# Optimization experiments

Measured on AMD Instinct MI355X. Metric: run time of the kernel, lower is better.

The kernel has to match this reference:

```python
import jax, jax.numpy as jnp
import numpy as np

SEQ_LEN = 720
PRED_LEN = 720
PERIOD = 24
EMB = 64
P_IN = SEQ_LEN // PERIOD            # 30
P_OUT = -(-PRED_LEN // PERIOD)      # 30 (ceil)
FREQ = EMB // 2 + 1                 # 33
DOM = (SEQ_LEN // PERIOD + 1) * 2 + 10  # 72
RATIO = PRED_LEN / SEQ_LEN          # 1.0


def _clin(z, Wr, Wi, br, bi):
    # complex nn.Linear over last dim: z @ W.T + b
    W = Wr + 1j * Wi
    b = br + 1j * bi
    return jnp.einsum('...i,oi->...o', z, W) + b


def _forward(x, freq_Wr, freq_Wi, freq_br, freq_bi, WP_W, WP_b, W_pos,
             mix1_Wr, mix1_Wi, mix1_br, mix1_bi,
             fmix_Wr, fmix_Wi, fmix_br, fmix_bi,
             proj_Wr, proj_Wi, proj_br, proj_bi,
             head_W, head_b):
    B, T, N = x.shape
    # ---- low-frequency branch ----
    low = jnp.fft.rfft(x, axis=1)[:, :DOM, :]               # [B, DOM, N] complex
    low = jnp.swapaxes(low, 1, 2)                           # [B, N, DOM]
    low = _clin(low, freq_Wr, freq_Wi, freq_br, freq_bi)    # [B, N, DOM_out]
    low = jnp.swapaxes(low, 1, 2)                           # [B, DOM_out, N]
    out_bins = PRED_LEN // 2 + 1
    low = jnp.pad(low, ((0, 0), (0, out_bins - low.shape[1]), (0, 0)))
    low_xy = jnp.fft.irfft(low, n=PRED_LEN, axis=1) * RATIO  # [B, PRED_LEN, N]

    # ---- period branch (single fixed period 24; SEQ_LEN % 24 == 0) ----
    xk = jnp.swapaxes(x, 1, 2).reshape(B, N, P_IN, PERIOD)  # unfold(size=step=24)
    xk = jnp.einsum('bnpi,oi->bnpo', xk, WP_W) + WP_b       # [B,N,P_IN,EMB]
    pf = jnp.fft.rfft(xk, axis=-1) + W_pos                  # [B,N,P_IN,FREQ] (W_pos real -> real part)
    pf = jnp.swapaxes(pf, -1, -2)                           # [B,N,FREQ,P_IN]
    o = _clin(pf, mix1_Wr, mix1_Wi, mix1_br, mix1_bi) + pf
    o = jnp.swapaxes(_clin(jnp.swapaxes(o, -1, -2), fmix_Wr, fmix_Wi, fmix_br, fmix_bi), -1, -2) + o
    o = _clin(o, proj_Wr, proj_Wi, proj_br, proj_bi)        # [B,N,FREQ,P_OUT]
    o = jnp.swapaxes(o, -1, -2)                             # [B,N,P_OUT,FREQ]
    pp = jnp.fft.irfft(o, n=EMB, axis=-1).reshape(B, N, P_OUT * EMB)
    pred = jnp.einsum('bnf,of->bno', pp, head_W) + head_b   # [B,N,PRED_LEN]
    pred = jnp.swapaxes(pred, 1, 2)                         # [B,PRED_LEN,N]
    return 0.7 * pred + 0.3 * low_xy


def setup_inputs() -> dict:
    B, N = 128, 128
    ks = jax.random.split(jax.random.key(0), 22)
    f32 = jnp.float32
    def w(k, shape, s=0.05):
        return jax.random.normal(k, shape, dtype=f32) * s
    return {
        'x': jax.random.normal(ks[0], (B, SEQ_LEN, N), dtype=f32),
        'freq_Wr': w(ks[1], (DOM, DOM)), 'freq_Wi': w(ks[2], (DOM, DOM)),
        'freq_br': w(ks[3], (DOM,)), 'freq_bi': w(ks[4], (DOM,)),
        'WP_W': w(ks[5], (EMB, PERIOD)), 'WP_b': w(ks[6], (EMB,)),
        'W_pos': jax.random.uniform(ks[7], (B, N, P_IN, FREQ), dtype=f32, minval=-0.02, maxval=0.02),
        'mix1_Wr': w(ks[8], (P_IN, P_IN)), 'mix1_Wi': w(ks[9], (P_IN, P_IN)),
        'mix1_br': w(ks[10], (P_IN,)), 'mix1_bi': w(ks[11], (P_IN,)),
        'fmix_Wr': w(ks[12], (FREQ, FREQ)), 'fmix_Wi': w(ks[13], (FREQ, FREQ)),
        'fmix_br': w(ks[14], (FREQ,)), 'fmix_bi': w(ks[15], (FREQ,)),
        'proj_Wr': w(ks[16], (P_OUT, P_IN)), 'proj_Wi': w(ks[17], (P_OUT, P_IN)),
        'proj_br': w(ks[18], (P_OUT,)), 'proj_bi': w(ks[19], (P_OUT,)),
        'head_W': w(ks[20], (PRED_LEN, P_OUT * EMB)), 'head_b': w(ks[21], (PRED_LEN,)),
    }


def reference(x, freq_Wr, freq_Wi, freq_br, freq_bi, WP_W, WP_b, W_pos,
              mix1_Wr, mix1_Wi, mix1_br, mix1_bi,
              fmix_Wr, fmix_Wi, fmix_br, fmix_bi,
              proj_Wr, proj_Wi, proj_br, proj_bi,
              head_W, head_b):
    return _forward(x, freq_Wr, freq_Wi, freq_br, freq_bi, WP_W, WP_b, W_pos,
                    mix1_Wr, mix1_Wi, mix1_br, mix1_bi,
                    fmix_Wr, fmix_Wi, fmix_br, fmix_bi,
                    proj_Wr, proj_Wi, proj_br, proj_bi,
                    head_W, head_b)
```

## Files before the change

kernel.cpp:

```cpp
#include <hip/hip_runtime.h>
#include <hip/hip_bf16.h>
#include <math.h>

#define SEQ 720
#define NCH 128
#define BATCH 128
#define BN 16384
#define DOM 72
#define PIN 30
#define POUT 30
#define FRQ 33
#define EMB 64
#define PER 24
#define KW 990
#define KP 1728
#define MT 768
#define PI_F 3.14159265358979323846f

typedef float2 cf;
typedef __attribute__((ext_vector_type(8))) short short8v;
__device__ __forceinline__ cf cmac(cf acc, cf a, cf b){
  acc.x += a.x*b.x - a.y*b.y; acc.y += a.x*b.y + a.y*b.x; return acc;
}
__device__ __forceinline__ short b2s(float f){
  __hip_bfloat16 h = __float2bfloat16(f);
  return *reinterpret_cast<short*>(&h);
}

__global__ __launch_bounds__(512) void fused_pre(
                         const float* __restrict__ WPW, const float* __restrict__ WPb,
                         const float* __restrict__ m1r, const float* __restrict__ m1i,
                         const float* __restrict__ m1br, const float* __restrict__ m1bi,
                         const float* __restrict__ fxr, const float* __restrict__ fxi,
                         const float* __restrict__ fxbr, const float* __restrict__ fxbi,
                         const float* __restrict__ pjr, const float* __restrict__ pji,
                         const float* __restrict__ pjbr, const float* __restrict__ pjbi,
                         const float* __restrict__ fqr, const float* __restrict__ fqi,
                         const float* __restrict__ x, const float* __restrict__ Wp,
                         cf* C, cf* PM, cf* M2, cf* o3b,
                         float* __restrict__ A1r, float* __restrict__ A1i,
                         __hip_bfloat16* __restrict__ Abig)
{
  __shared__ double arena_d[5900];
  char* smem = (char*)arena_d;
  int tid = threadIdx.x;
  int blk = blockIdx.x;

  if (blk < DOM){
    cf* tbl  = (cf*)(smem);
    cf* wrow = (cf*)(smem + 5760);
    int k = blk;
    for (int m=tid;m<720;m+=512){ float s,c; sincosf(-2.f*PI_F*(float)m/720.f,&s,&c); tbl[m]=make_float2(c,s); }
    for (int j=tid;j<DOM;j+=512) wrow[j]=make_float2(fqr[k*DOM+j], fqi[k*DOM+j]);
    __syncthreads();
    for (int tau=tid; tau<720; tau+=512){
      cf acc=make_float2(0.f,0.f);
      for (int j=0;j<DOM;++j) acc = cmac(acc, wrow[j], tbl[(j*tau)%720]);
      A1r[k*720+tau]=acc.x;
      A1i[k*720+tau]=acc.y;
    }
    return;
  }

  if (blk == DOM){
    cf*    e64  = (cf*)(smem + 0);
    float* sW   = (float*)(smem + 512);
    float* sWb  = (float*)(smem + 6656);
    float* sM1r = (float*)(smem + 6912);
    float* sM1i = (float*)(smem + 10512);
    float* sFxr = (float*)(smem + 14112);
    float* sFxi = (float*)(smem + 18468);
    float* sPjr = (float*)(smem + 22824);
    float* sPji = (float*)(smem + 26424);
    float* sB   = (float*)(smem + 30024);
    cf*    s_d  = (cf*)(smem + 30816);
    cf*    s_rs = (cf*)(smem + 31080);
    cf*    s_o1 = (cf*)(smem + 31320);
    cf*    s_o2 = (cf*)(smem + 39240);
    if (tid < 64){ float s,c; sincosf(2.f*PI_F*tid/64.f, &s, &c); e64[tid] = make_float2(c, s); }
    for (int i=tid; i<EMB*PER; i+=512) sW[i]=WPW[i];
    if (tid < EMB) sWb[tid]=WPb[tid];
    for (int i=tid; i<PIN*PIN; i+=512){ sM1r[i]=m1r[i]; sM1i[i]=m1i[i]; sPjr[i]=pjr[i]; sPji[i]=pji[i]; }
    for (int i=tid; i<FRQ*FRQ; i+=512){ sFxr[i]=fxr[i]; sFxi[i]=fxi[i]; }
    if (tid < PIN)  { sB[tid]      = m1br[tid]; sB[33+tid]  = m1bi[tid]; }
    if (tid < FRQ)  { sB[66+tid]   = fxbr[tid]; sB[99+tid]  = fxbi[tid]; }
    if (tid < POUT) { sB[132+tid]  = pjbr[tid]; sB[165+tid] = pjbi[tid]; }
    __syncthreads();
    for (int idx=tid; idx<FRQ*PER; idx+=512){
      int f = idx/PER, i = idx%PER;
      cf acc = make_float2(0.f,0.f);
      #pragma unroll 8
      for (int o=0;o<EMB;++o){ cf e = e64[(f*o)&63]; float w = sW[o*PER+i]; acc.x += w*e.x; acc.y -= w*e.y; }
      C[idx] = acc;
    }
    for (int f=tid; f<FRQ; f+=512){
      cf acc = make_float2(0.f,0.f);
      #pragma unroll 8
      for (int o=0;o<EMB;++o){ cf e = e64[(f*o)&63]; acc.x += sWb[o]*e.x; acc.y -= sWb[o]*e.y; }
      s_d[f]=acc;
    }
    for (int idx=tid; idx<POUT*PIN; idx+=512){
      int q = idx/PIN, pp = idx%PIN;
      cf acc = make_float2(sPjr[q*PIN+pp], sPji[q*PIN+pp]);
      #pragma unroll 6
      for (int p=0;p<PIN;++p){
        cf a = make_float2(sPjr[q*PIN+p], sPji[q*PIN+p]);
        cf b = make_float2(sM1r[p*PIN+pp], sM1i[p*PIN+pp]);
        acc = cmac(acc, a, b);
      }
      PM[idx]=acc;
    }
    for (int idx=tid; idx<FRQ*FRQ; idx+=512){
      int f = idx/FRQ, ff = idx%FRQ;
      cf v = make_float2(sFxr[idx], sFxi[idx]); if (f==ff) v.x += 1.f;
      M2[idx]=v;
    }
    for (int p=tid; p<PIN; p+=512){
      cf acc = make_float2(1.f,0.f);
      #pragma unroll 6
      for (int pp=0;pp<PIN;++pp){ acc.x += sM1r[p*PIN+pp]; acc.y += sM1i[p*PIN+pp]; }
      s_rs[p]=acc;
    }
    __syncthreads();
    for (int idx=tid; idx<FRQ*PIN; idx+=512){
      int f = idx/PIN, p = idx%PIN;
      cf v = make_float2(0.f,0.f); v = cmac(v, s_d[f], s_rs[p]);
      v.x += sB[p]; v.y += sB[33+p];
      s_o1[idx]=v;
    }
    __syncthreads();
    for (int idx=tid; idx<FRQ*PIN; idx+=512){
      int f = idx/PIN, p = idx%PIN;
      cf acc = make_float2(sB[66+f], sB[99+f]);
      #pragma unroll 4
      for (int ff=0; ff<FRQ; ++ff){
        cf m2 = make_float2(sFxr[f*FRQ+ff], sFxi[f*FRQ+ff]); if (f==ff) m2.x += 1.f;
        acc = cmac(acc, m2, s_o1[ff*PIN+p]);
      }
      s_o2[idx]=acc;
    }
    __syncthreads();
    for (int idx=tid; idx<FRQ*POUT; idx+=512){
      int f = idx/POUT, q = idx%POUT;
      cf acc = make_float2(sB[132+q], sB[165+q]);
      #pragma unroll 6
      for (int p=0;p<PIN;++p){
        cf a = make_float2(sPjr[q*PIN+p], sPji[q*PIN+p]);
        acc = cmac(acc, a, s_o2[f*PIN+p]);
      }
      o3b[f*POUT+q]=acc;
    }
    return;
  }

  if (blk < DOM + 1 + 3072){
    float (*tile)[68] = (float(*)[68])smem;
    int bb = blk - (DOM+1);
    int b = bb/24; int rem = bb%24;
    int t0 = (rem>>1)*64, n0 = (rem&1)*64;
    int r0 = tid >> 4;
    int c4 = (tid & 15)*4;
    #pragma unroll
    for (int s=0;s<2;++s){
      int r = r0 + s*32;
      int t = t0 + r;
      float4 v = make_float4(0.f,0.f,0.f,0.f);
      if (t < SEQ) v = *reinterpret_cast<const float4*>(&x[((size_t)b*SEQ + t)*NCH + n0 + c4]);
      *reinterpret_cast<float4*>(&tile[r][c4]) = v;
    }
    __syncthreads();
    int n  = tid & 63;
    int tg = tid >> 6;
    int tt = tg*8;
    if (t0 + tt < SEQ){
      short8v v;
      #pragma unroll
      for (int j=0;j<8;++j) v[j] = b2s(tile[tt+j][n]);
      *reinterpret_cast<short8v*>(Abig + (size_t)(b*NCH + n0+n)*KP + t0 + tt) = v;
    }
    return;
  }

  {
    int bb = blk - (DOM+1) - 3072;
    int lane8 = tid >> 6;
    int bn = bb*8 + lane8;
    int j = (tid & 63)*4;
    const float* src = Wp + (size_t)bn*KW;
    __hip_bfloat16* dstb = Abig + (size_t)bn*KP + SEQ;
    for (int jj = j; jj < KP-SEQ; jj += 256){
      float f0,f1,f2,f3;
      if (jj+3 < KW){
        float2 u = *reinterpret_cast<const float2*>(src+jj);
        float2 w = *reinterpret_cast<const float2*>(src+jj+2);
        f0=u.x; f1=u.y; f2=w.x; f3=w.y;
      } else {
        f0=(jj  <KW)?src[jj  ]:0.f; f1=(jj+1<KW)?src[jj+1]:0.f;
        f2=(jj+2<KW)?src[jj+2]:0.f; f3=(jj+3<KW)?src[jj+3]:0.f;
      }
      short4 v = { b2s(f0), b2s(f1), b2s(f2), b2s(f3) };
      *reinterpret_cast<short4*>(dstb + jj) = v;
    }
  }
}

__global__ __launch_bounds__(512) void p_big3(const float* __restrict__ hW,
                    const cf* __restrict__ PM, const cf* __restrict__ M2, const cf* __restrict__ o3b,
                    const cf* __restrict__ Cm,
                    const float* __restrict__ fbr, const float* __restrict__ fbi,
                    const float* __restrict__ headb,
                    const float* __restrict__ A1r, const float* __restrict__ A1i,
                    __hip_bfloat16* __restrict__ BTm, float* __restrict__ bias){
  __shared__ double smem_d[6336];
  char* smem = (char*)smem_d;
  int tid = threadIdx.x;
  cf*    e64 = (cf*)(smem + 0);
  float* shw = (float*)(smem + 512);
  cf*    sHc = (cf*)(smem + 8192);
  cf*    sV1 = (cf*)(smem + 16112);
  cf*    sPM = (cf*)(smem + 24032);
  cf*    sM2 = (cf*)(smem + 31232);
  cf*    sO3 = (cf*)(smem + 39944);
  float* red = (float*)(smem + 47864);
  float* sG  = (float*)(smem + 49912);
  cf* sC = (cf*)shw;
  cf* sV = sHc;
  int t = blockIdx.x;
  if (tid<64){ float s,c; sincosf(2.f*PI_F*tid/64.f,&s,&c); e64[tid]=make_float2(c,s); }
  if (tid<DOM){
    int m=(tid*t)%720; float s,c; sincosf(2.f*PI_F*(float)m/720.f,&s,&c);
    float sc=(tid==0)?(1.f/720.f):(2.f/720.f);
    sG[tid]=c*sc; sG[72+tid]=s*sc;
  }
  for (int i=tid;i<1920;i+=512) shw[i]=hW[(size_t)t*1920+i];
  for (int i=tid;i<POUT*PIN;i+=512) sPM[i]=PM[i];
  for (int i=tid;i<FRQ*FRQ;i+=512) sM2[i]=M2[i];
  for (int i=tid;i<FRQ*POUT;i+=512) sO3[i]=o3b[i];
  __syncthreads();
  for (int idx=tid; idx<990; idx+=512){
    int q=idx/FRQ, f=idx%FRQ;
    cf acc=make_float2(0.f,0.f);
    const float* hw = &shw[q*64];
    #pragma unroll 8
    for (int o=0;o<EMB;++o){ cf e=e64[(f*o)&63]; float w=hw[o]; acc.x+=w*e.x; acc.y+=w*e.y; }
    float s=((f==0)||(f==32))?(1.f/64.f):(2.f/64.f);
    sHc[idx]=make_float2(acc.x*s, acc.y*s);
  }
  __syncthreads();
  for (int idx=tid; idx<990; idx+=512){
    int f=idx/PIN, p=idx%PIN;
    cf acc=make_float2(0.f,0.f);
    #pragma unroll 6
    for (int q=0;q<POUT;++q) acc=cmac(acc, sHc[q*FRQ+f], sPM[q*PIN+p]);
    sV1[idx]=acc;
  }
  float part=0.f;
  for (int idx=tid; idx<990; idx+=512){
    int q=idx/FRQ, f=idx%FRQ;
    cf h=sHc[idx]; cf o=sO3[f*POUT+q];
    part += h.x*o.x - h.y*o.y;
  }
  part *= 0.7f;
  if (tid<DOM){
    int m=(tid*t)%720; float s,c; sincosf(2.f*PI_F*(float)m/720.f,&s,&c);
    float sc=(tid==0)?(1.f/720.f):(2.f/720.f);
    part += 0.3f*sc*(c*fbr[tid] - s*fbi[tid]);
  }
  for (int i=tid;i<FRQ*PER;i+=512) sC[i]=Cm[i];
  red[tid]=part; __syncthreads();
  for (int s=256;s>0;s>>=1){ if (tid<s) red[tid]+=red[tid+s]; __syncthreads(); }
  if (tid==0) bias[t] = red[0] + 0.7f*headb[t];
  __syncthreads();
  for (int idx=tid; idx<990; idx+=512){
    int ff=idx/PIN, pp=idx%PIN;
    cf acc=make_float2(0.f,0.f);
    #pragma unroll 4
    for (int f=0;f<FRQ;++f) acc=cmac(acc, sV1[f*PIN+pp], sM2[f*FRQ+ff]);
    sV[idx]=acc;
  }
  __syncthreads();
  for (int tau=tid; tau<720; tau+=512){
    int p0 = tau/PER, i0 = tau - p0*PER;
    float mper=0.f;
    #pragma unroll 4
    for (int f=0; f<FRQ; ++f){ cf v=sV[f*PIN+p0]; cf c=sC[f*PER+i0]; mper += v.x*c.x - v.y*c.y; }
    float mlow=0.f;
    #pragma unroll 8
    for (int k=0;k<DOM;++k)
      mlow += sG[k]*A1r[k*720+tau] - sG[72+k]*A1i[k*720+tau];
    BTm[(size_t)t*KP + tau] = __float2bfloat16(0.3f*mlow + 0.7f*mper);
  }
  for (int j=tid;j<KP-SEQ;j+=512){
    float v = 0.f;
    if (j < KW){ int p=j/FRQ, f=j-p*FRQ; v = 0.7f * sV[f*PIN+p].x; }
    BTm[(size_t)t*KP + SEQ + j] = __float2bfloat16(v);
  }
}

typedef __attribute__((ext_vector_type(8))) short bfrag_t;
typedef __attribute__((ext_vector_type(4))) float accf_t;
typedef __attribute__((address_space(1))) void gvoid;
typedef __attribute__((address_space(3))) void lvoid;

__device__ __forceinline__ void gload16(const void* g, void* l){
  __builtin_amdgcn_global_load_lds((gvoid*)(g), (lvoid*)(l), 16, 0, 0);
}

__global__ __launch_bounds__(512, 6) void gemm_main(const __hip_bfloat16* __restrict__ BTm,
                                                    const __hip_bfloat16* __restrict__ Abig,
                                                    const float* __restrict__ bias,
                                                    float* __restrict__ out)
{
  __shared__ __hip_bfloat16 At[128*32];
  __shared__ __hip_bfloat16 Bt[128*32];
  int tid = threadIdx.x;
  int lane = tid & 63;
  int wv = tid >> 6;
  int wr = wv >> 1, wc = wv & 1;
  int t0 = blockIdx.y*128, bn0 = blockIdx.x*128;

  accf_t acc[2][4];
  #pragma unroll
  for (int i=0;i<2;++i)
    #pragma unroll
    for (int j=0;j<4;++j) acc[i][j] = (accf_t){0.f,0.f,0.f,0.f};

  int row = tid >> 2, u = tid & 3;
  int ug = u ^ ((row>>1)&3);
  const __hip_bfloat16* gA = BTm  + (size_t)(t0 + row)*KP + ug*8;
  const __hip_bfloat16* gB = Abig + (size_t)(bn0+ row)*KP + ug*8;
  char* lA = (char*)At + tid*16;
  char* lB = (char*)Bt + tid*16;

  int g = lane>>4;
  int arowb = wr*32 + (lane&15);
  int browb = wc*64 + (lane&15);

  for (int ks=0; ks<KP/32; ++ks){
    int k0 = ks*32;
    gload16(gA + k0, lA);
    gload16(gB + k0, lB);
    __syncthreads();
    bfrag_t af[2], bb[4];
    #pragma unroll
    for (int mi=0;mi<2;++mi){
      int r = arowb + mi*16;
      int uu = g ^ ((r>>1)&3);
      af[mi] = *(const bfrag_t*)((const char*)At + r*64 + uu*16);
    }
    #pragma unroll
    for (int ni=0;ni<4;++ni){
      int r = browb + ni*16;
      int uu = g ^ ((r>>1)&3);
      bb[ni] = *(const bfrag_t*)((const char*)Bt + r*64 + uu*16);
    }
    #pragma unroll
    for (int mi=0;mi<2;++mi)
      #pragma unroll
      for (int ni=0;ni<4;++ni)
        acc[mi][ni] = __builtin_amdgcn_mfma_f32_16x16x32_bf16(af[mi], bb[ni], acc[mi][ni], 0, 0, 0);
    __syncthreads();
  }

  #pragma unroll
  for (int mi=0;mi<2;++mi){
    int tbase = t0 + wr*32 + mi*16 + (lane>>4)*4;
    #pragma unroll
    for (int ni=0;ni<4;++ni){
      int col = bn0 + wc*64 + ni*16 + (lane&15);
      int b = col>>7, n = col&127;
      size_t obase = (size_t)b*(SEQ*NCH) + n;
      #pragma unroll
      for (int r=0;r<4;++r){
        int t = tbase + r;
        if (t<SEQ) out[obase + (size_t)t*NCH] = acc[mi][ni][r] + bias[t];
      }
    }
  }
}

extern "C" void kernel_launch(void* const* d_in, const int* in_sizes, int n_in,
                              void* d_out, int out_size, void* d_ws, size_t ws_size,
                              hipStream_t stream)
{
  const float* x     = (const float*)d_in[0];
  const float* fqWr  = (const float*)d_in[1];
  const float* fqWi  = (const float*)d_in[2];
  const float* fqbr  = (const float*)d_in[3];
  const float* fqbi  = (const float*)d_in[4];
  const float* WPW   = (const float*)d_in[5];
  const float* WPb   = (const float*)d_in[6];
  const float* Wpos  = (const float*)d_in[7];
  const float* m1r   = (const float*)d_in[8];
  const float* m1i   = (const float*)d_in[9];
  const float* m1br  = (const float*)d_in[10];
  const float* m1bi  = (const float*)d_in[11];
  const float* fxr   = (const float*)d_in[12];
  const float* fxi   = (const float*)d_in[13];
  const float* fxbr  = (const float*)d_in[14];
  const float* fxbi  = (const float*)d_in[15];
  const float* pjr   = (const float*)d_in[16];
  const float* pji   = (const float*)d_in[17];
  const float* pjbr  = (const float*)d_in[18];
  const float* pjbi  = (const float*)d_in[19];
  const float* headW = (const float*)d_in[20];
  const float* headb = (const float*)d_in[21];

  char* ws = (char*)d_ws;
  size_t off = 0;
  auto alloc = [&](size_t bytes)->void*{ void* p = ws + off; off += (bytes + 255) & ~(size_t)255; return p; };
  __hip_bfloat16* Abig = (__hip_bfloat16*)alloc((size_t)BN*KP*2);
  __hip_bfloat16* BTm  = (__hip_bfloat16*)alloc((size_t)MT*KP*2);
  float* A1r = (float*)alloc((size_t)DOM*720*4);
  float* A1i = (float*)alloc((size_t)DOM*720*4);
  cf* C   = (cf*)alloc((size_t)FRQ*PER*8);
  cf* PM  = (cf*)alloc((size_t)POUT*PIN*8);
  cf* M2  = (cf*)alloc((size_t)FRQ*FRQ*8);
  cf* o3b = (cf*)alloc((size_t)FRQ*POUT*8);
  float* bias = (float*)alloc((size_t)SEQ*4);

  fused_pre<<<DOM+1+3072+2048,512,0,stream>>>(WPW,WPb, m1r,m1i,m1br,m1bi, fxr,fxi,fxbr,fxbi,
                                              pjr,pji,pjbr,pjbi, fqWr,fqWi, x, Wpos,
                                              C,PM,M2,o3b, A1r,A1i, Abig);
  p_big3<<<SEQ,512,0,stream>>>(headW, PM, M2, o3b, C, fqbr, fqbi, headb, A1r, A1i, BTm, bias);
  gemm_main<<<dim3(128, 6), 512, 0, stream>>>(BTm, Abig, bias, (float*)d_out);
}
```

Before: 129.4 us.

## Fuse per-timestep weight build with input conversion into one interleaved kernel

Splits the single-block parameter precompute into its own tiny kernel. The per-output-row weight construction (formerly p_big3) is merged into the large bf16 conversion kernel, with every eighth block doing row work so the compute-heavy blocks interleave with the memory-bound transpose and convert blocks. The low-frequency DFT matrix A1 is no longer materialized: each row folds the frequency weights into a 72-term vector gw and evaluates the DFT directly through a twiddle table. This removes one launch and the A1 global traffic, but each row block now does extra sincos and gw work, and the tiny p1_only kernel stays serialized ahead of everything.

```diff
diff --git a/kernel.cpp b/kernel.cpp
--- a/kernel.cpp
+++ b/kernel.cpp
@@ -27,7 +27,7 @@
   return *reinterpret_cast<short*>(&h);
 }
 
-__global__ __launch_bounds__(512) void fused_pre(
+__global__ __launch_bounds__(512) void p1_only(
                          const float* __restrict__ WPW, const float* __restrict__ WPb,
                          const float* __restrict__ m1r, const float* __restrict__ m1i,
                          const float* __restrict__ m1br, const float* __restrict__ m1bi,
@@ -35,128 +35,219 @@
                          const float* __restrict__ fxbr, const float* __restrict__ fxbi,
                          const float* __restrict__ pjr, const float* __restrict__ pji,
                          const float* __restrict__ pjbr, const float* __restrict__ pjbi,
-                         const float* __restrict__ fqr, const float* __restrict__ fqi,
-                         const float* __restrict__ x, const float* __restrict__ Wp,
-                         cf* C, cf* PM, cf* M2, cf* o3b,
-                         float* __restrict__ A1r, float* __restrict__ A1i,
-                         __hip_bfloat16* __restrict__ Abig)
+                         cf* C, cf* PM, cf* M2, cf* o3b)
 {
   __shared__ double arena_d[5900];
   char* smem = (char*)arena_d;
   int tid = threadIdx.x;
+  cf*    e64  = (cf*)(smem + 0);
+  float* sW   = (float*)(smem + 512);
+  float* sWb  = (float*)(smem + 6656);
+  float* sM1r = (float*)(smem + 6912);
+  float* sM1i = (float*)(smem + 10512);
+  float* sFxr = (float*)(smem + 14112);
+  float* sFxi = (float*)(smem + 18468);
+  float* sPjr = (float*)(smem + 22824);
+  float* sPji = (float*)(smem + 26424);
+  float* sB   = (float*)(smem + 30024);
+  cf*    s_d  = (cf*)(smem + 30816);
+  cf*    s_rs = (cf*)(smem + 31080);
+  cf*    s_o1 = (cf*)(smem + 31320);
+  cf*    s_o2 = (cf*)(smem + 39240);
+  if (tid < 64){ float s,c; sincosf(2.f*PI_F*tid/64.f, &s, &c); e64[tid] = make_float2(c, s); }
+  for (int i=tid; i<EMB*PER; i+=512) sW[i]=WPW[i];
+  if (tid < EMB) sWb[tid]=WPb[tid];
+  for (int i=tid; i<PIN*PIN; i+=512){ sM1r[i]=m1r[i]; sM1i[i]=m1i[i]; sPjr[i]=pjr[i]; sPji[i]=pji[i]; }
+  for (int i=tid; i<FRQ*FRQ; i+=512){ sFxr[i]=fxr[i]; sFxi[i]=fxi[i]; }
+  if (tid < PIN)  { sB[tid]      = m1br[tid]; sB[33+tid]  = m1bi[tid]; }
+  if (tid < FRQ)  { sB[66+tid]   = fxbr[tid]; sB[99+tid]  = fxbi[tid]; }
+  if (tid < POUT) { sB[132+tid]  = pjbr[tid]; sB[165+tid] = pjbi[tid]; }
+  __syncthreads();
+  for (int idx=tid; idx<FRQ*PER; idx+=512){
+    int f = idx/PER, i = idx%PER;
+    cf acc = make_float2(0.f,0.f);
+    #pragma unroll 8
+    for (int o=0;o<EMB;++o){ cf e = e64[(f*o)&63]; float w = sW[o*PER+i]; acc.x += w*e.x; acc.y -= w*e.y; }
+    C[idx] = acc;
+  }
+  for (int f=tid; f<FRQ; f+=512){
+    cf acc = make_float2(0.f,0.f);
+    #pragma unroll 8
+    for (int o=0;o<EMB;++o){ cf e = e64[(f*o)&63]; acc.x += sWb[o]*e.x; acc.y -= sWb[o]*e.y; }
+    s_d[f]=acc;
+  }
+  for (int idx=tid; idx<POUT*PIN; idx+=512){
+    int q = idx/PIN, pp = idx%PIN;
+    cf acc = make_float2(sPjr[q*PIN+pp], sPji[q*PIN+pp]);
+    #pragma unroll 6
+    for (int p=0;p<PIN;++p){
+      cf a = make_float2(sPjr[q*PIN+p], sPji[q*PIN+p]);
+      cf b = make_float2(sM1r[p*PIN+pp], sM1i[p*PIN+pp]);
+      acc = cmac(acc, a, b);
+    }
+    PM[idx]=acc;
+  }
+  for (int idx=tid; idx<FRQ*FRQ; idx+=512){
+    int f = idx/FRQ, ff = idx%FRQ;
+    cf v = make_float2(sFxr[idx], sFxi[idx]); if (f==ff) v.x += 1.f;
+    M2[idx]=v;
+  }
+  for (int p=tid; p<PIN; p+=512){
+    cf acc = make_float2(1.f,0.f);
+    #pragma unroll 6
+    for (int pp=0;pp<PIN;++pp){ acc.x += sM1r[p*PIN+pp]; acc.y += sM1i[p*PIN+pp]; }
+    s_rs[p]=acc;
+  }
+  __syncthreads();
+  for (int idx=tid; idx<FRQ*PIN; idx+=512){
+    int f = idx/PIN, p = idx%PIN;
+    cf v = make_float2(0.f,0.f); v = cmac(v, s_d[f], s_rs[p]);
+    v.x += sB[p]; v.y += sB[33+p];
+    s_o1[idx]=v;
+  }
+  __syncthreads();
+  for (int idx=tid; idx<FRQ*PIN; idx+=512){
+    int f = idx/PIN, p = idx%PIN;
+    cf acc = make_float2(sB[66+f], sB[99+f]);
+    #pragma unroll 4
+    for (int ff=0; ff<FRQ; ++ff){
+      cf m2 = make_float2(sFxr[f*FRQ+ff], sFxi[f*FRQ+ff]); if (f==ff) m2.x += 1.f;
+      acc = cmac(acc, m2, s_o1[ff*PIN+p]);
+    }
+    s_o2[idx]=acc;
+  }
+  __syncthreads();
+  for (int idx=tid; idx<FRQ*POUT; idx+=512){
+    int f = idx/POUT, q = idx%POUT;
+    cf acc = make_float2(sB[132+q], sB[165+q]);
+    #pragma unroll 6
+    for (int p=0;p<PIN;++p){
+      cf a = make_float2(sPjr[q*PIN+p], sPji[q*PIN+p]);
+      acc = cmac(acc, a, s_o2[f*PIN+p]);
+    }
+    o3b[f*POUT+q]=acc;
+  }
+}
+
+__global__ __launch_bounds__(512) void mega(const float* __restrict__ hW,
+                    const cf* __restrict__ PM, const cf* __restrict__ M2, const cf* __restrict__ o3b,
+                    const cf* __restrict__ Cm,
+                    const float* __restrict__ fqr, const float* __restrict__ fqi,
+                    const float* __restrict__ fbr, const float* __restrict__ fbi,
+                    const float* __restrict__ headb,
+                    const float* __restrict__ x, const float* __restrict__ Wp,
+                    __hip_bfloat16* __restrict__ BTm, float* __restrict__ bias,
+                    __hip_bfloat16* __restrict__ Abig){
+  __shared__ double smem_d[6336];
+  char* smem = (char*)smem_d;
+  int tid = threadIdx.x;
   int blk = blockIdx.x;
 
-  if (blk < DOM){
-    cf* tbl  = (cf*)(smem);
-    cf* wrow = (cf*)(smem + 5760);
-    int k = blk;
-    for (int m=tid;m<720;m+=512){ float s,c; sincosf(-2.f*PI_F*(float)m/720.f,&s,&c); tbl[m]=make_float2(c,s); }
-    for (int j=tid;j<DOM;j+=512) wrow[j]=make_float2(fqr[k*DOM+j], fqi[k*DOM+j]);
+  bool isP4 = ((blk & 7) == 0) && (blk < 5760);
+  if (isP4){
+    cf*    e64 = (cf*)(smem + 0);
+    float* shw = (float*)(smem + 512);
+    cf*    sHc = (cf*)(smem + 8192);
+    cf*    sV1 = (cf*)(smem + 16112);
+    cf*    sPM = (cf*)(smem + 24032);
+    cf*    sM2 = (cf*)(smem + 31232);
+    cf*    sO3 = (cf*)(smem + 39944);
+    float* red = (float*)(smem + 47864);
+    cf*    gw  = (cf*)(smem + 49912);
+    cf* sC = (cf*)shw;
+    cf* sV = sHc;
+    cf* tbl = sPM;
+    int t = blk >> 3;
+    if (tid<64){ float s,c; sincosf(2.f*PI_F*tid/64.f,&s,&c); e64[tid]=make_float2(c,s); }
+    for (int i=tid;i<1920;i+=512) shw[i]=hW[(size_t)t*1920+i];
+    for (int i=tid;i<POUT*PIN;i+=512) sPM[i]=PM[i];
+    for (int i=tid;i<FRQ*FRQ;i+=512) sM2[i]=M2[i];
+    for (int i=tid;i<FRQ*POUT;i+=512) sO3[i]=o3b[i];
+    if (tid < DOM){
+      int j = tid;
+      cf acc = make_float2(0.f,0.f);
+      for (int k=0;k<DOM;++k){
+        int m=(k*t)%720; float s,c; sincosf(2.f*PI_F*(float)m/720.f,&s,&c);
+        float sc=(k==0)?(1.f/720.f):(2.f/720.f);
+        float wr = fqr[k*DOM+j], wi = fqi[k*DOM+j];
+        acc.x += sc*(c*wr - s*wi);
+        acc.y += sc*(c*wi + s*wr);
+      }
+      gw[j] = acc;
+    }
+    __syncthreads();
+    for (int idx=tid; idx<990; idx+=512){
+      int q=idx/FRQ, f=idx%FRQ;
+      cf acc=make_float2(0.f,0.f);
+      const float* hw = &shw[q*64];
+      #pragma unroll 8
+      for (int o=0;o<EMB;++o){ cf e=e64[(f*o)&63]; float w=hw[o]; acc.x+=w*e.x; acc.y+=w*e.y; }
+      float s=((f==0)||(f==32))?(1.f/64.f):(2.f/64.f);
+      sHc[idx]=make_float2(acc.x*s, acc.y*s);
+    }
+    __syncthreads();
+    for (int idx=tid; idx<990; idx+=512){
+      int f=idx/PIN, p=idx%PIN;
+      cf acc=make_float2(0.f,0.f);
+      #pragma unroll 6
+      for (int q=0;q<POUT;++q) acc=cmac(acc, sHc[q*FRQ+f], sPM[q*PIN+p]);
+      sV1[idx]=acc;
+    }
+    float part=0.f;
+    for (int idx=tid; idx<990; idx+=512){
+      int q=idx/FRQ, f=idx%FRQ;
+      cf h=sHc[idx]; cf o=sO3[f*POUT+q];
+      part += h.x*o.x - h.y*o.y;
+    }
+    part *= 0.7f;
+    if (tid<DOM){
+      int m=(tid*t)%720; float s,c; sincosf(2.f*PI_F*(float)m/720.f,&s,&c);
+      float sc=(tid==0)?(1.f/720.f):(2.f/720.f);
+      part += 0.3f*sc*(c*fbr[tid] - s*fbi[tid]);
+    }
+    for (int i=tid;i<FRQ*PER;i+=512) sC[i]=Cm[i];
+    red[tid]=part; __syncthreads();
+    for (int s=256;s>0;s>>=1){ if (tid<s) red[tid]+=red[tid+s]; __syncthreads(); }
+    if (tid==0) bias[t] = red[0] + 0.7f*headb[t];
+    __syncthreads();
+    for (int idx=tid; idx<990; idx+=512){
+      int ff=idx/PIN, pp=idx%PIN;
+      cf acc=make_float2(0.f,0.f);
+      #pragma unroll 4
+      for (int f=0;f<FRQ;++f) acc=cmac(acc, sV1[f*PIN+pp], sM2[f*FRQ+ff]);
+      sV[idx]=acc;
+    }
+    for (int m=tid;m<720;m+=512){
+      float s,c; sincosf(2.f*PI_F*(float)m/720.f,&s,&c);
+      tbl[m]=make_float2(c,s);
+    }
     __syncthreads();
     for (int tau=tid; tau<720; tau+=512){
-      cf acc=make_float2(0.f,0.f);
-      for (int j=0;j<DOM;++j) acc = cmac(acc, wrow[j], tbl[(j*tau)%720]);
-      A1r[k*720+tau]=acc.x;
-      A1i[k*720+tau]=acc.y;
+      int p0 = tau/PER, i0 = tau - p0*PER;
+      float mper=0.f;
+      #pragma unroll 4
+      for (int f=0; f<FRQ; ++f){ cf v=sV[f*PIN+p0]; cf c=sC[f*PER+i0]; mper += v.x*c.x - v.y*c.y; }
+      float mlow=0.f;
+      #pragma unroll 8
+      for (int j=0;j<DOM;++j){
+        cf g = gw[j]; cf e = tbl[(j*tau)%720];
+        mlow += g.x*e.x + g.y*e.y;
+      }
+      BTm[(size_t)t*KP + tau] = __float2bfloat16(0.3f*mlow + 0.7f*mper);
+    }
+    for (int j=tid;j<KP-SEQ;j+=512){
+      float v = 0.f;
+      if (j < KW){ int p=j/FRQ, f=j-p*FRQ; v = 0.7f * sV[f*PIN+p].x; }
+      BTm[(size_t)t*KP + SEQ + j] = __float2bfloat16(v);
     }
     return;
   }
 
-  if (blk == DOM){
-    cf*    e64  = (cf*)(smem + 0);
-    float* sW   = (float*)(smem + 512);
-    float* sWb  = (float*)(smem + 6656);
-    float* sM1r = (float*)(smem + 6912);
-    float* sM1i = (float*)(smem + 10512);
-    float* sFxr = (float*)(smem + 14112);
-    float* sFxi = (float*)(smem + 18468);
-    float* sPjr = (float*)(smem + 22824);
-    float* sPji = (float*)(smem + 26424);
-    float* sB   = (float*)(smem + 30024);
-    cf*    s_d  = (cf*)(smem + 30816);
-    cf*    s_rs = (cf*)(smem + 31080);
-    cf*    s_o1 = (cf*)(smem + 31320);
-    cf*    s_o2 = (cf*)(smem + 39240);
-    if (tid < 64){ float s,c; sincosf(2.f*PI_F*tid/64.f, &s, &c); e64[tid] = make_float2(c, s); }
-    for (int i=tid; i<EMB*PER; i+=512) sW[i]=WPW[i];
-    if (tid < EMB) sWb[tid]=WPb[tid];
-    for (int i=tid; i<PIN*PIN; i+=512){ sM1r[i]=m1r[i]; sM1i[i]=m1i[i]; sPjr[i]=pjr[i]; sPji[i]=pji[i]; }
-    for (int i=tid; i<FRQ*FRQ; i+=512){ sFxr[i]=fxr[i]; sFxi[i]=fxi[i]; }
-    if (tid < PIN)  { sB[tid]      = m1br[tid]; sB[33+tid]  = m1bi[tid]; }
-    if (tid < FRQ)  { sB[66+tid]   = fxbr[tid]; sB[99+tid]  = fxbi[tid]; }
-    if (tid < POUT) { sB[132+tid]  = pjbr[tid]; sB[165+tid] = pjbi[tid]; }
-    __syncthreads();
-    for (int idx=tid; idx<FRQ*PER; idx+=512){
-      int f = idx/PER, i = idx%PER;
-      cf acc = make_float2(0.f,0.f);
-      #pragma unroll 8
-      for (int o=0;o<EMB;++o){ cf e = e64[(f*o)&63]; float w = sW[o*PER+i]; acc.x += w*e.x; acc.y -= w*e.y; }
-      C[idx] = acc;
-    }
-    for (int f=tid; f<FRQ; f+=512){
-      cf acc = make_float2(0.f,0.f);
-      #pragma unroll 8
-      for (int o=0;o<EMB;++o){ cf e = e64[(f*o)&63]; acc.x += sWb[o]*e.x; acc.y -= sWb[o]*e.y; }
-      s_d[f]=acc;
-    }
-    for (int idx=tid; idx<POUT*PIN; idx+=512){
-      int q = idx/PIN, pp = idx%PIN;
-      cf acc = make_float2(sPjr[q*PIN+pp], sPji[q*PIN+pp]);
-      #pragma unroll 6
-      for (int p=0;p<PIN;++p){
-        cf a = make_float2(sPjr[q*PIN+p], sPji[q*PIN+p]);
-        cf b = make_float2(sM1r[p*PIN+pp], sM1i[p*PIN+pp]);
-        acc = cmac(acc, a, b);
-      }
-      PM[idx]=acc;
-    }
-    for (int idx=tid; idx<FRQ*FRQ; idx+=512){
-      int f = idx/FRQ, ff = idx%FRQ;
-      cf v = make_float2(sFxr[idx], sFxi[idx]); if (f==ff) v.x += 1.f;
-      M2[idx]=v;
-    }
-    for (int p=tid; p<PIN; p+=512){
-      cf acc = make_float2(1.f,0.f);
-      #pragma unroll 6
-      for (int pp=0;pp<PIN;++pp){ acc.x += sM1r[p*PIN+pp]; acc.y += sM1i[p*PIN+pp]; }
-      s_rs[p]=acc;
-    }
-    __syncthreads();
-    for (int idx=tid; idx<FRQ*PIN; idx+=512){
-      int f = idx/PIN, p = idx%PIN;
-      cf v = make_float2(0.f,0.f); v = cmac(v, s_d[f], s_rs[p]);
-      v.x += sB[p]; v.y += sB[33+p];
-      s_o1[idx]=v;
-    }
-    __syncthreads();
-    for (int idx=tid; idx<FRQ*PIN; idx+=512){
-      int f = idx/PIN, p = idx%PIN;
-      cf acc = make_float2(sB[66+f], sB[99+f]);
-      #pragma unroll 4
-      for (int ff=0; ff<FRQ; ++ff){
-        cf m2 = make_float2(sFxr[f*FRQ+ff], sFxi[f*FRQ+ff]); if (f==ff) m2.x += 1.f;
-        acc = cmac(acc, m2, s_o1[ff*PIN+p]);
-      }
-      s_o2[idx]=acc;
-    }
-    __syncthreads();
-    for (int idx=tid; idx<FRQ*POUT; idx+=512){
-      int f = idx/POUT, q = idx%POUT;
-      cf acc = make_float2(sB[132+q], sB[165+q]);
-      #pragma unroll 6
-      for (int p=0;p<PIN;++p){
-        cf a = make_float2(sPjr[q*PIN+p], sPji[q*PIN+p]);
-        acc = cmac(acc, a, s_o2[f*PIN+p]);
-      }
-      o3b[f*POUT+q]=acc;
-    }
-    return;
-  }
-
-  if (blk < DOM + 1 + 3072){
+  int rid = (blk < 5760) ? (blk - (blk>>3) - 1) : (blk - 720);
+
+  if (rid < 3072){
     float (*tile)[68] = (float(*)[68])smem;
-    int bb = blk - (DOM+1);
-    int b = bb/24; int rem = bb%24;
+    int b = rid/24; int rem = rid%24;
     int t0 = (rem>>1)*64, n0 = (rem&1)*64;
     int r0 = tid >> 4;
     int c4 = (tid & 15)*4;
@@ -182,7 +273,7 @@
   }
 
   {
-    int bb = blk - (DOM+1) - 3072;
+    int bb = rid - 3072;
     int lane8 = tid >> 6;
     int bn = bb*8 + lane8;
     int j = (tid & 63)*4;
@@ -201,99 +292,6 @@
       short4 v = { b2s(f0), b2s(f1), b2s(f2), b2s(f3) };
       *reinterpret_cast<short4*>(dstb + jj) = v;
     }
-  }
-}
-
-__global__ __launch_bounds__(512) void p_big3(const float* __restrict__ hW,
-                    const cf* __restrict__ PM, const cf* __restrict__ M2, const cf* __restrict__ o3b,
-                    const cf* __restrict__ Cm,
-                    const float* __restrict__ fbr, const float* __restrict__ fbi,
-                    const float* __restrict__ headb,
-                    const float* __restrict__ A1r, const float* __restrict__ A1i,
-                    __hip_bfloat16* __restrict__ BTm, float* __restrict__ bias){
-  __shared__ double smem_d[6336];
-  char* smem = (char*)smem_d;
-  int tid = threadIdx.x;
-  cf*    e64 = (cf*)(smem + 0);
-  float* shw = (float*)(smem + 512);
-  cf*    sHc = (cf*)(smem + 8192);
-  cf*    sV1 = (cf*)(smem + 16112);
-  cf*    sPM = (cf*)(smem + 24032);
-  cf*    sM2 = (cf*)(smem + 31232);
-  cf*    sO3 = (cf*)(smem + 39944);
-  float* red = (float*)(smem + 47864);
-  float* sG  = (float*)(smem + 49912);
-  cf* sC = (cf*)shw;
-  cf* sV = sHc;
-  int t = blockIdx.x;
-  if (tid<64){ float s,c; sincosf(2.f*PI_F*tid/64.f,&s,&c); e64[tid]=make_float2(c,s); }
-  if (tid<DOM){
-    int m=(tid*t)%720; float s,c; sincosf(2.f*PI_F*(float)m/720.f,&s,&c);
-    float sc=(tid==0)?(1.f/720.f):(2.f/720.f);
-    sG[tid]=c*sc; sG[72+tid]=s*sc;
-  }
-  for (int i=tid;i<1920;i+=512) shw[i]=hW[(size_t)t*1920+i];
-  for (int i=tid;i<POUT*PIN;i+=512) sPM[i]=PM[i];
-  for (int i=tid;i<FRQ*FRQ;i+=512) sM2[i]=M2[i];
-  for (int i=tid;i<FRQ*POUT;i+=512) sO3[i]=o3b[i];
-  __syncthreads();
-  for (int idx=tid; idx<990; idx+=512){
-    int q=idx/FRQ, f=idx%FRQ;
-    cf acc=make_float2(0.f,0.f);
-    const float* hw = &shw[q*64];
-    #pragma unroll 8
-    for (int o=0;o<EMB;++o){ cf e=e64[(f*o)&63]; float w=hw[o]; acc.x+=w*e.x; acc.y+=w*e.y; }
-    float s=((f==0)||(f==32))?(1.f/64.f):(2.f/64.f);
-    sHc[idx]=make_float2(acc.x*s, acc.y*s);
-  }
-  __syncthreads();
-  for (int idx=tid; idx<990; idx+=512){
-    int f=idx/PIN, p=idx%PIN;
-    cf acc=make_float2(0.f,0.f);
-    #pragma unroll 6
-    for (int q=0;q<POUT;++q) acc=cmac(acc, sHc[q*FRQ+f], sPM[q*PIN+p]);
-    sV1[idx]=acc;
-  }
-  float part=0.f;
-  for (int idx=tid; idx<990; idx+=512){
-    int q=idx/FRQ, f=idx%FRQ;
-    cf h=sHc[idx]; cf o=sO3[f*POUT+q];
-    part += h.x*o.x - h.y*o.y;
-  }
-  part *= 0.7f;
-  if (tid<DOM){
-    int m=(tid*t)%720; float s,c; sincosf(2.f*PI_F*(float)m/720.f,&s,&c);
-    float sc=(tid==0)?(1.f/720.f):(2.f/720.f);
-    part += 0.3f*sc*(c*fbr[tid] - s*fbi[tid]);
-  }
-  for (int i=tid;i<FRQ*PER;i+=512) sC[i]=Cm[i];
-  red[tid]=part; __syncthreads();
-  for (int s=256;s>0;s>>=1){ if (tid<s) red[tid]+=red[tid+s]; __syncthreads(); }
-  if (tid==0) bias[t] = red[0] + 0.7f*headb[t];
-  __syncthreads();
-  for (int idx=tid; idx<990; idx+=512){
-    int ff=idx/PIN, pp=idx%PIN;
-    cf acc=make_float2(0.f,0.f);
-    #pragma unroll 4
-    for (int f=0;f<FRQ;++f) acc=cmac(acc, sV1[f*PIN+pp], sM2[f*FRQ+ff]);
-    sV[idx]=acc;
-  }
-  __syncthreads();
-  for (int tau=tid; tau<720; tau+=512){
-    int p0 = tau/PER, i0 = tau - p0*PER;
-    float mper=0.f;
-    #pragma unroll 4
-    for (int f=0; f<FRQ; ++f){ cf v=sV[f*PIN+p0]; cf c=sC[f*PER+i0]; mper += v.x*c.x - v.y*c.y; }
-    float mlow=0.f;
-    #pragma unroll 8
-    for (int k=0;k<DOM;++k)
-      mlow += sG[k]*A1r[k*720+tau] - sG[72+k]*A1i[k*720+tau];
-    BTm[(size_t)t*KP + tau] = __float2bfloat16(0.3f*mlow + 0.7f*mper);
-  }
-  for (int j=tid;j<KP-SEQ;j+=512){
-    float v = 0.f;
-    if (j < KW){ int p=j/FRQ, f=j-p*FRQ; v = 0.7f * sV[f*PIN+p].x; }
-    BTm[(size_t)t*KP + SEQ + j] = __float2bfloat16(v);
   }
 }
 
@@ -411,17 +409,15 @@
   auto alloc = [&](size_t bytes)->void*{ void* p = ws + off; off += (bytes + 255) & ~(size_t)255; return p; };
   __hip_bfloat16* Abig = (__hip_bfloat16*)alloc((size_t)BN*KP*2);
   __hip_bfloat16* BTm  = (__hip_bfloat16*)alloc((size_t)MT*KP*2);
-  float* A1r = (float*)alloc((size_t)DOM*720*4);
-  float* A1i = (float*)alloc((size_t)DOM*720*4);
   cf* C   = (cf*)alloc((size_t)FRQ*PER*8);
   cf* PM  = (cf*)alloc((size_t)POUT*PIN*8);
   cf* M2  = (cf*)alloc((size_t)FRQ*FRQ*8);
   cf* o3b = (cf*)alloc((size_t)FRQ*POUT*8);
   float* bias = (float*)alloc((size_t)SEQ*4);
 
-  fused_pre<<<DOM+1+3072+2048,512,0,stream>>>(WPW,WPb, m1r,m1i,m1br,m1bi, fxr,fxi,fxbr,fxbi,
-                                              pjr,pji,pjbr,pjbi, fqWr,fqWi, x, Wpos,
-                                              C,PM,M2,o3b, A1r,A1i, Abig);
-  p_big3<<<SEQ,512,0,stream>>>(headW, PM, M2, o3b, C, fqbr, fqbi, headb, A1r, A1i, BTm, bias);
+  p1_only<<<1,512,0,stream>>>(WPW,WPb, m1r,m1i,m1br,m1bi, fxr,fxi,fxbr,fxbi,
+                              pjr,pji,pjbr,pjbi, C,PM,M2,o3b);
+  mega<<<5840,512,0,stream>>>(headW, PM, M2, o3b, C, fqWr, fqWi, fqbr, fqbi, headb,
+                              x, Wpos, BTm, bias, Abig);
   gemm_main<<<dim3(128, 6), 512, 0, stream>>>(BTm, Abig, bias, (float*)d_out);
 }
```

New measurement: 444.5 us. 3.43x slower.
